# Performance work log

Hardware: AMD Instinct MI355X
Metric: run time of the kernel (lower is better)

The kernel has to match this reference:

```python
import jax, jax.numpy as jnp
import numpy as np

VOCAB, EMB, HID, TAG, T = 500000, 50, 50, 5, 4096  # HID = hidden_dim//2 per direction
START, STOP, NEG = 3, 4, -10000.0


def setup_inputs() -> dict:
    key = jax.random.key(0)
    ks = jax.random.split(key, 14)
    sentence = jax.random.randint(ks[0], (T,), 0, VOCAB, dtype=jnp.int32)
    embed = jax.random.normal(ks[1], (VOCAB, EMB), dtype=jnp.float32)
    # PyTorch LSTM params, gate order (i, f, g, o); b = b_ih + b_hh fused (same math)
    Wih_f = jax.random.normal(ks[2], (4 * HID, EMB), dtype=jnp.float32) * 0.1
    Whh_f = jax.random.normal(ks[3], (4 * HID, HID), dtype=jnp.float32) * 0.1
    b_f = jax.random.normal(ks[4], (4 * HID,), dtype=jnp.float32) * 0.1
    Wih_b = jax.random.normal(ks[5], (4 * HID, EMB), dtype=jnp.float32) * 0.1
    Whh_b = jax.random.normal(ks[6], (4 * HID, HID), dtype=jnp.float32) * 0.1
    b_b = jax.random.normal(ks[7], (4 * HID,), dtype=jnp.float32) * 0.1
    Wt = jax.random.normal(ks[8], (TAG, 2 * HID), dtype=jnp.float32) * 0.1
    bt = jax.random.normal(ks[9], (TAG,), dtype=jnp.float32) * 0.1
    transitions = jax.random.normal(ks[10], (TAG, TAG), dtype=jnp.float32)
    transitions = transitions.at[START, :].set(NEG).at[:, STOP].set(NEG)
    h0 = jax.random.normal(ks[11], (2, HID), dtype=jnp.float32)  # [fwd/bwd dir]
    c0 = jax.random.normal(ks[12], (2, HID), dtype=jnp.float32)
    return dict(sentence=sentence, embed=embed, Wih_f=Wih_f, Whh_f=Whh_f, b_f=b_f,
                Wih_b=Wih_b, Whh_b=Whh_b, b_b=b_b, Wt=Wt, bt=bt,
                transitions=transitions, h0=h0, c0=c0)


def _lstm_dir(x, h0, c0, Wih, Whh, b):
    # x: [T, EMB] -> hs: [T, HID]; PyTorch gate order i,f,g,o
    def step(carry, xt):
        h, c = carry
        z = xt @ Wih.T + h @ Whh.T + b  # [4H]
        i, f, g, o = jnp.split(z, 4)
        i, f, o = jax.nn.sigmoid(i), jax.nn.sigmoid(f), jax.nn.sigmoid(o)
        c = f * c + i * jnp.tanh(g)
        h = o * jnp.tanh(c)
        return (h, c), h
    _, hs = jax.lax.scan(step, (h0, c0), x)
    return hs


def _lstm_feats(sentence, embed, Wih_f, Whh_f, b_f, Wih_b, Whh_b, b_b, Wt, bt, h0, c0):
    x = embed[sentence]                       # [T, EMB]
    hf = _lstm_dir(x, h0[0], c0[0], Wih_f, Whh_f, b_f)            # [T, HID]
    hb = _lstm_dir(x[::-1], h0[1], c0[1], Wih_b, Whh_b, b_b)[::-1]  # [T, HID]
    h = jnp.concatenate([hf, hb], axis=-1)    # [T, 2*HID]
    return h @ Wt.T + bt                       # [T, TAG]


def reference(sentence, embed, Wih_f, Whh_f, b_f, Wih_b, Whh_b, b_b, Wt, bt, transitions, h0, c0):
    feats = _lstm_feats(sentence, embed, Wih_f, Whh_f, b_f, Wih_b, Whh_b, b_b, Wt, bt, h0, c0)

    fv0 = jnp.full((TAG,), NEG, dtype=feats.dtype).at[START].set(0.0)

    def vstep(fv, feat):
        m = fv[None, :] + transitions          # [next_tag, prev_tag]
        bp = jnp.argmax(m, axis=1)             # [TAG] best prev for each next
        fv_new = jnp.max(m, axis=1) + feat
        return fv_new, bp

    fv, bps = jax.lax.scan(vstep, fv0, feats)  # bps: [T, TAG]
    terminal = fv + transitions[STOP]
    last = jnp.argmax(terminal)

    def bt_step(tag, bp):
        return bp[tag], tag                    # carry prev tag, emit current tag

    _start, path = jax.lax.scan(bt_step, last, bps, reverse=True)
    score = terminal[last]
    return path.astype(jnp.int32), score
```

## Files before the change

kernel.cpp:

```cpp
#include <hip/hip_runtime.h>
#include <math.h>

#define EMB 50
#define HID 50
#define G4  200
#define NTAG 5
#define NEGV (-10000.0f)
#define TAG_START 3
#define TAG_STOP  4
#define T_MAX 4096
#define TB 8
#define WPAD 52

typedef float f32x4 __attribute__((ext_vector_type(4)));
typedef float f32x2 __attribute__((ext_vector_type(2)));

#define LO2(v) __builtin_shufflevector(v, v, 0, 1)
#define HI2(v) __builtin_shufflevector(v, v, 2, 3)

__global__ __launch_bounds__(256)
void k_embed_proj(const int* __restrict__ sent,
                  const float* __restrict__ embed,
                  const float* __restrict__ Wf, const float* __restrict__ bf,
                  const float* __restrict__ Wb, const float* __restrict__ bb,
                  float* __restrict__ pre, int T) {
  __shared__ __align__(16) float Wl[G4 * WPAD];
  __shared__ __align__(16) float xl[TB * WPAD];
  const int tid = threadIdx.x;
  const int t0  = blockIdx.x * TB;
  int ntt = T - t0; if (ntt > TB) ntt = TB;

  for (int e = tid; e < ntt * EMB; e += 256) {
    int tt = e / EMB, k = e - tt * EMB;
    xl[tt * WPAD + k] = embed[(long long)sent[t0 + tt] * EMB + k];
  }

  for (int ph = 0; ph < 2; ++ph) {
    const float* W = ph ? Wb : Wf;
    const float* b = ph ? bb : bf;
    __syncthreads();
    for (int e = tid; e < G4 * EMB; e += 256) {
      int r = e / EMB, k = e - r * EMB;
      Wl[r * WPAD + k] = W[e];
    }
    __syncthreads();
    float* outBase = pre + ((long long)ph * (T + 4) + 2) * G4;
    for (int o = tid; o < ntt * G4; o += 256) {
      int tt = o / G4, j = o - tt * G4;
      const float* wr_ = &Wl[j * WPAD];
      const float* xx  = &xl[tt * WPAD];
      f32x2 a2 = {0.f, 0.f};
#pragma unroll
      for (int k4 = 0; k4 < 12; ++k4) {
        f32x4 wv = *(const f32x4*)&wr_[4 * k4];
        f32x4 xv = *(const f32x4*)&xx[4 * k4];
        a2 += LO2(wv) * LO2(xv);
        a2 += HI2(wv) * HI2(xv);
      }
      a2.x += wr_[48] * xx[48];
      a2.y += wr_[49] * xx[49];
      float acc = b[j] + a2.x + a2.y;
      int unit = j % HID, gate = j / HID;
      outBase[(long long)(t0 + tt) * G4 + unit * 4 + gate] = acc;
    }
  }
}

#define DPP_XOR1(v) __int_as_float(__builtin_amdgcn_update_dpp(0, __float_as_int(v), 0xB1, 0xF, 0xF, true))
#define DPP_XOR2(v) __int_as_float(__builtin_amdgcn_update_dpp(0, __float_as_int(v), 0x4E, 0xF, 0xF, true))
#define DPP_XOR3(v) __int_as_float(__builtin_amdgcn_update_dpp(0, __float_as_int(v), 0x1B, 0xF, 0xF, true))

__device__ __forceinline__ float dot16(f32x4 w0, f32x4 w1, f32x4 w2, f32x4 w3,
                                       f32x4 x0, f32x4 x1, f32x4 x2, f32x4 x3) {
  f32x2 a = {0.f, 0.f}, b = {0.f, 0.f};
  a += LO2(w0) * LO2(x0);  b += HI2(w0) * HI2(x0);
  a += LO2(w1) * LO2(x1);  b += HI2(w1) * HI2(x1);
  a += LO2(w2) * LO2(x2);  b += HI2(w2) * HI2(x2);
  a += LO2(w3) * LO2(x3);  b += HI2(w3) * HI2(x3);
  return (a.x + b.x) + (a.y + b.y);
}

#define LSTM_STEP(HRbuf, HWbuf)                                              \
  {                                                                          \
    const float* HR = HRbuf;                                                 \
    float*       HW = HWbuf;                                                 \
    f32x4 mp = *(const f32x4*)pp;                                            \
    pp += sG4;                                                               \
    f32x4 x0 = *(const f32x4*)&HR[16 * q + 0];                               \
    f32x4 x1 = *(const f32x4*)&HR[16 * q + 4];                               \
    f32x4 x2 = *(const f32x4*)&HR[16 * q + 8];                               \
    f32x4 x3 = *(const f32x4*)&HR[16 * q + 12];                              \
    float pi = dot16(Wi0, Wi1, Wi2, Wi3, x0, x1, x2, x3);                    \
    float pf = dot16(Wf0, Wf1, Wf2, Wf3, x0, x1, x2, x3);                    \
    float pg = dot16(Wg0, Wg1, Wg2, Wg3, x0, x1, x2, x3);                    \
    float po = dot16(Wo0, Wo1, Wo2, Wo3, x0, x1, x2, x3);                    \
    pi += DPP_XOR1(pi); pi += DPP_XOR2(pi);                                  \
    pf += DPP_XOR1(pf); pf += DPP_XOR2(pf);                                  \
    pg += DPP_XOR1(pg); pg += DPP_XOR2(pg);                                  \
    po += DPP_XOR1(po); po += DPP_XOR2(po);                                  \
    float zi = cp.x + pi, zf = cp.y + pf, zg = cp.z + pg, zo = cp.w + po;    \
    float zq = (q == 0) ? zi : (q == 1) ? zf : (q == 2) ? zg : zo;           \
    float xs = (q == 2) ? 2.f * zq : zq;                                     \
    float eq = __expf(-xs);                                                  \
    float sg = __builtin_amdgcn_rcpf(1.f + eq);                              \
    float act = (q == 2) ? 2.f * sg - 1.f : sg;                              \
    float ga1 = DPP_XOR1(act);                                               \
    float ga2 = DPP_XOR2(act);                                               \
    float ga3 = DPP_XOR3(act);                                               \
    float iv = (q == 0) ? act : (q == 1) ? ga1 : (q == 2) ? ga2 : ga3;       \
    float fv = (q == 0) ? ga1 : (q == 1) ? act : (q == 2) ? ga3 : ga2;       \
    float gv = (q == 0) ? ga2 : (q == 1) ? ga3 : (q == 2) ? act : ga1;       \
    float ov = (q == 0) ? ga3 : (q == 1) ? ga2 : (q == 2) ? ga1 : act;       \
    c = fv * c + iv * gv;                                                    \
    float e2 = __expf(-2.f * c);                                             \
    float tc = 2.f * __builtin_amdgcn_rcpf(1.f + e2) - 1.f;                  \
    float h = ov * tc;                                                       \
    if (wr) {                                                                \
      HW[jq] = h;                                                            \
      *hsp = h;                                                              \
    }                                                                        \
    asm volatile("s_waitcnt lgkmcnt(0)\n\ts_barrier" ::: "memory");          \
    hsp += sH;                                                               \
    cp = np; np = mp;                                                        \
  }

__global__ __launch_bounds__(256)
__attribute__((amdgpu_waves_per_eu(1, 1)))
void k_lstm(const float* __restrict__ pre,
            const float* __restrict__ Whh_f,
            const float* __restrict__ Whh_b,
            const float* __restrict__ h0, const float* __restrict__ c0,
            float* __restrict__ hs, int T) {
  const int d   = blockIdx.x;
  const int tid = threadIdx.x;
  const int j   = tid >> 2;
  const int q   = tid & 3;
  const int jq  = (j < HID) ? j : 0;
  const bool wr = (q == 0) && (j < HID);
  const float* __restrict__ Whh  = d ? Whh_b : Whh_f;
  const float* __restrict__ preD = pre + ((long long)d * (T + 4) + 2) * G4;

  __shared__ __align__(16) float hA[64];
  __shared__ __align__(16) float hB[64];

  const float* p0 = Whh + (long long)(0 * HID + jq) * HID + 16 * q;
  const float* p1 = Whh + (long long)(1 * HID + jq) * HID + 16 * q;
  const float* p2 = Whh + (long long)(2 * HID + jq) * HID + 16 * q;
  const float* p3 = Whh + (long long)(3 * HID + jq) * HID + 16 * q;
  f32x4 Wi0, Wi1, Wi2, Wi3, Wf0, Wf1, Wf2, Wf3;
  f32x4 Wg0, Wg1, Wg2, Wg3, Wo0, Wo1, Wo2, Wo3;
  asm volatile(
      "global_load_dwordx4 %0,  %16, off\n\t"
      "global_load_dwordx4 %1,  %16, off offset:16\n\t"
      "global_load_dwordx4 %2,  %16, off offset:32\n\t"
      "global_load_dwordx4 %3,  %16, off offset:48\n\t"
      "global_load_dwordx4 %4,  %17, off\n\t"
      "global_load_dwordx4 %5,  %17, off offset:16\n\t"
      "global_load_dwordx4 %6,  %17, off offset:32\n\t"
      "global_load_dwordx4 %7,  %17, off offset:48\n\t"
      "global_load_dwordx4 %8,  %18, off\n\t"
      "global_load_dwordx4 %9,  %18, off offset:16\n\t"
      "global_load_dwordx4 %10, %18, off offset:32\n\t"
      "global_load_dwordx4 %11, %18, off offset:48\n\t"
      "global_load_dwordx4 %12, %19, off\n\t"
      "global_load_dwordx4 %13, %19, off offset:16\n\t"
      "global_load_dwordx4 %14, %19, off offset:32\n\t"
      "global_load_dwordx4 %15, %19, off offset:48\n\t"
      "s_waitcnt vmcnt(0)"
      : "=&v"(Wi0), "=&v"(Wi1), "=&v"(Wi2), "=&v"(Wi3),
        "=&v"(Wf0), "=&v"(Wf1), "=&v"(Wf2), "=&v"(Wf3),
        "=&v"(Wg0), "=&v"(Wg1), "=&v"(Wg2), "=&v"(Wg3),
        "=&v"(Wo0), "=&v"(Wo1), "=&v"(Wo2), "=&v"(Wo3)
      : "v"(p0), "v"(p1), "v"(p2), "v"(p3));

  if (q == 3) {
    const f32x4 z4 = {0.f, 0.f, 0.f, 0.f};
    Wi0.z = 0.f; Wi0.w = 0.f; Wi1 = z4; Wi2 = z4; Wi3 = z4;
    Wf0.z = 0.f; Wf0.w = 0.f; Wf1 = z4; Wf2 = z4; Wf3 = z4;
    Wg0.z = 0.f; Wg0.w = 0.f; Wg1 = z4; Wg2 = z4; Wg3 = z4;
    Wo0.z = 0.f; Wo0.w = 0.f; Wo1 = z4; Wo2 = z4; Wo3 = z4;
  }

  float c = c0[d * HID + jq];
  if (tid < 64) { hA[tid] = 0.f; hB[tid] = 0.f; }
  __syncthreads();
  if (wr) hA[jq] = h0[d * HID + jq];
  __syncthreads();

  const int s = d ? -1 : 1;
  const int t0 = d ? (T - 1) : 0;
  const long long sG4 = (long long)s * G4;
  const long long sH  = (long long)s * (2 * HID);

  f32x4 cp = *(const f32x4*)&preD[(long long)t0 * G4 + 4 * jq];
  f32x4 np = *(const f32x4*)&preD[(long long)(t0 + s) * G4 + 4 * jq];
  const float* pp = preD + (long long)(t0 + 2 * s) * G4 + 4 * jq;
  float* hsp = hs + (long long)t0 * (2 * HID) + d * HID + jq;

  for (int it = 0; it < T; it += 2) {
    LSTM_STEP(hA, hB)
    LSTM_STEP(hB, hA)
  }
}

__global__ void k_feats(const float* __restrict__ hs, const float* __restrict__ Wt,
                        const float* __restrict__ bt, float* __restrict__ feats, int T) {
  int g = blockIdx.x * blockDim.x + threadIdx.x;
  if (g >= T * NTAG) return;
  int t = g / NTAG, m = g % NTAG;
  const float* h = hs + (long long)t * (2 * HID);
  const float* w = Wt + m * (2 * HID);
  float a = bt[m];
#pragma unroll
  for (int k = 0; k < 2 * HID; ++k) a += w[k] * h[k];
  feats[g] = a;
}

__global__ __launch_bounds__(64, 1)
void k_vchunk(const float* __restrict__ feats,
              const float* __restrict__ trans,
              float* __restrict__ fvh, float* __restrict__ misc,
              float* __restrict__ out, int T) {
  const int lane = threadIdx.x;
  const int L    = T >> 6;
  const int c0   = lane * L;

  __shared__ float Pl[64][26];

  float tr[NTAG * NTAG];
#pragma unroll
  for (int i = 0; i < NTAG * NTAG; ++i) tr[i] = trans[i];

  float P[25];
  {
    float ft[5];
#pragma unroll
    for (int k = 0; k < 5; ++k) ft[k] = feats[c0 * 5 + k];
#pragma unroll
    for (int n = 0; n < 5; ++n)
#pragma unroll
      for (int p = 0; p < 5; ++p) P[n * 5 + p] = tr[n * 5 + p] + ft[n];
  }
  for (int i = 1; i < L; ++i) {
    int t = c0 + i;
    float ft[5];
#pragma unroll
    for (int k = 0; k < 5; ++k) ft[k] = feats[t * 5 + k];
    float NP[25];
#pragma unroll
    for (int n = 0; n < 5; ++n) {
#pragma unroll
      for (int p = 0; p < 5; ++p) {
        float m = tr[n * 5 + 0] + P[0 + p];
        m = fmaxf(m, tr[n * 5 + 1] + P[5 + p]);
        m = fmaxf(m, tr[n * 5 + 2] + P[10 + p]);
        m = fmaxf(m, tr[n * 5 + 3] + P[15 + p]);
        m = fmaxf(m, tr[n * 5 + 4] + P[20 + p]);
        NP[n * 5 + p] = m + ft[n];
      }
    }
#pragma unroll
    for (int e = 0; e < 25; ++e) P[e] = NP[e];
  }
#pragma unroll
  for (int e = 0; e < 25; ++e) Pl[lane][e] = P[e];
  __syncthreads();

  float v0 = NEGV, v1 = NEGV, v2 = NEGV, v3 = 0.f, v4 = NEGV;
  float s0 = 0.f, s1 = 0.f, s2 = 0.f, s3 = 0.f, s4 = 0.f;
  for (int cc = 0; cc < 64; ++cc) {
    bool mine = (cc == lane);
    s0 = mine ? v0 : s0; s1 = mine ? v1 : s1; s2 = mine ? v2 : s2;
    s3 = mine ? v3 : s3; s4 = mine ? v4 : s4;
    float nv[5];
#pragma unroll
    for (int n = 0; n < 5; ++n) {
      float m = Pl[cc][n * 5 + 0] + v0;
      m = fmaxf(m, Pl[cc][n * 5 + 1] + v1);
      m = fmaxf(m, Pl[cc][n * 5 + 2] + v2);
      m = fmaxf(m, Pl[cc][n * 5 + 3] + v3);
      m = fmaxf(m, Pl[cc][n * 5 + 4] + v4);
      nv[n] = m;
    }
    v0 = nv[0]; v1 = nv[1]; v2 = nv[2]; v3 = nv[3]; v4 = nv[4];
  }

  float f0 = s0, f1 = s1, f2 = s2, f3 = s3, f4 = s4;
  for (int i = 0; i < L; ++i) {
    int t = c0 + i;
    fvh[t * 5 + 0] = f0; fvh[t * 5 + 1] = f1; fvh[t * 5 + 2] = f2;
    fvh[t * 5 + 3] = f3; fvh[t * 5 + 4] = f4;
    float ft0 = feats[t * 5 + 0], ft1 = feats[t * 5 + 1], ft2 = feats[t * 5 + 2];
    float ft3 = feats[t * 5 + 3], ft4 = feats[t * 5 + 4];
    float n0 = fmaxf(fmaxf(fmaxf(f0 + tr[0],  f1 + tr[1]),  fmaxf(f2 + tr[2],  f3 + tr[3])),  f4 + tr[4])  + ft0;
    float n1 = fmaxf(fmaxf(fmaxf(f0 + tr[5],  f1 + tr[6]),  fmaxf(f2 + tr[7],  f3 + tr[8])),  f4 + tr[9])  + ft1;
    float n2 = fmaxf(fmaxf(fmaxf(f0 + tr[10], f1 + tr[11]), fmaxf(f2 + tr[12], f3 + tr[13])), f4 + tr[14]) + ft2;
    float n3 = fmaxf(fmaxf(fmaxf(f0 + tr[15], f1 + tr[16]), fmaxf(f2 + tr[17], f3 + tr[18])), f4 + tr[19]) + ft3;
    float n4 = fmaxf(fmaxf(fmaxf(f0 + tr[20], f1 + tr[21]), fmaxf(f2 + tr[22], f3 + tr[23])), f4 + tr[24]) + ft4;
    f0 = n0; f1 = n1; f2 = n2; f3 = n3; f4 = n4;
  }

  if (lane == 63) {
    float b0 = f0 + tr[TAG_STOP * 5 + 0], b1 = f1 + tr[TAG_STOP * 5 + 1];
    float b2 = f2 + tr[TAG_STOP * 5 + 2], b3 = f3 + tr[TAG_STOP * 5 + 3];
    float b4 = f4 + tr[TAG_STOP * 5 + 4];
    int last = 0; float best = b0;
    if (b1 > best) { best = b1; last = 1; }
    if (b2 > best) { best = b2; last = 2; }
    if (b3 > best) { best = b3; last = 3; }
    if (b4 > best) { best = b4; last = 4; }
    out[T] = best; misc[0] = (float)last;
  }
}

__global__ __launch_bounds__(1024) void k_vbt(const float* __restrict__ trans,
                        const float* __restrict__ fvh, const float* __restrict__ misc,
                        float* __restrict__ out, int T) {
  __shared__ unsigned int bufA[T_MAX];
  __shared__ unsigned int bufB[T_MAX];
  int tid = threadIdx.x;

  {
    float tr[NTAG * NTAG];
#pragma unroll
    for (int i = 0; i < NTAG * NTAG; ++i) tr[i] = trans[i];
    for (int t = tid; t < T; t += 1024) {
      unsigned pack;
      if (t == T - 1) {
        pack = 0u | (1u << 3) | (2u << 6) | (3u << 9) | (4u << 12);
      } else {
        const float* fv = fvh + (long long)(t + 1) * 5;
        float g0 = fv[0], g1 = fv[1], g2 = fv[2], g3 = fv[3], g4 = fv[4];
        pack = 0u;
#pragma unroll
        for (int nx = 0; nx < NTAG; ++nx) {
          float v0 = g0 + tr[nx * 5 + 0], v1 = g1 + tr[nx * 5 + 1], v2 = g2 + tr[nx * 5 + 2];
          float v3 = g3 + tr[nx * 5 + 3], v4 = g4 + tr[nx * 5 + 4];
          int bi = 0; float bv = v0;
          if (v1 > bv) { bv = v1; bi = 1; }
          if (v2 > bv) { bv = v2; bi = 2; }
          if (v3 > bv) { bv = v3; bi = 3; }
          if (v4 > bv) { bv = v4; bi = 4; }
          pack |= (unsigned)bi << (3 * nx);
        }
      }
      bufA[t] = pack;
    }
  }
  __syncthreads();

  unsigned int* cur = bufA;
  unsigned int* nxt = bufB;
  for (int dstep = 1; dstep < T; dstep <<= 1) {
    for (int t = tid; t < T; t += 1024) {
      unsigned v = cur[t];
      int u = t + dstep;
      if (u < T) {
        unsigned qq_ = cur[u];
        unsigned r = 0u;
#pragma unroll
        for (int x = 0; x < NTAG; ++x) {
          unsigned qs = (qq_ >> (3 * x)) & 7u;
          unsigned pp = (v >> (3 * qs)) & 7u;
          r |= pp << (3 * x);
        }
        v = r;
      }
      nxt[t] = v;
    }
    __syncthreads();
    unsigned int* tmp = cur; cur = nxt; nxt = tmp;
  }

  int last = (int)misc[0];
  for (int t = tid; t < T; t += 1024) {
    out[t] = (float)((cur[t] >> (3 * last)) & 7u);
  }
}

extern "C" void kernel_launch(void* const* d_in, const int* in_sizes, int n_in,
                              void* d_out, int out_size, void* d_ws, size_t ws_size,
                              hipStream_t stream) {
  const int*   sent  = (const int*)  d_in[0];
  const float* embed = (const float*)d_in[1];
  const float* Wih_f = (const float*)d_in[2];
  const float* Whh_f = (const float*)d_in[3];
  const float* b_f   = (const float*)d_in[4];
  const float* Wih_b = (const float*)d_in[5];
  const float* Whh_b = (const float*)d_in[6];
  const float* b_b   = (const float*)d_in[7];
  const float* Wt    = (const float*)d_in[8];
  const float* bt    = (const float*)d_in[9];
  const float* trans = (const float*)d_in[10];
  const float* h0    = (const float*)d_in[11];
  const float* c0    = (const float*)d_in[12];
  int T = in_sizes[0];

  float* out = (float*)d_out;
  float* pre   = (float*)d_ws;
  float* hs    = pre + 2 * (size_t)(T + 4) * G4;
  float* feats = hs + (size_t)T * 2 * HID;
  float* fvh   = feats + (size_t)T * NTAG;
  float* misc  = fvh + (size_t)(T + 1) * NTAG;

  k_embed_proj<<<(T + TB - 1) / TB, 256, 0, stream>>>(sent, embed, Wih_f, b_f, Wih_b, b_b, pre, T);
  k_lstm<<<2, 256, 0, stream>>>(pre, Whh_f, Whh_b, h0, c0, hs, T);
  k_feats<<<(T * NTAG + 255) / 256, 256, 0, stream>>>(hs, Wt, bt, feats, T);
  k_vchunk<<<1, 64, 0, stream>>>(feats, trans, fvh, misc, out, T);
  k_vbt<<<1, 1024, 0, stream>>>(trans, fvh, misc, out, T);
}
```

Measured before the change: 1.425 ms.

## Run each LSTM direction in a single wavefront, dropping barriers and DPP reductions

The recurrent LSTM kernel moves from 256 threads, with four lanes per hidden unit joined by DPP reductions and an s_barrier every step, to a single 64-lane wavefront. In the new layout each lane holds all four full 50-wide weight rows in registers and computes every gate itself. Because the whole block is one wave, the shared h vector is written and read with no hardware barrier. The per-step gate exchange and the tanh of the g gate are simplified as well, reusing exp(-z) squared. In exchange each lane does about four times more multiply-adds per step and needs many more registers.

```diff
diff --git a/kernel.cpp b/kernel.cpp
--- a/kernel.cpp
+++ b/kernel.cpp
@@ -66,140 +66,106 @@
   }
 }
 
-#define DPP_XOR1(v) __int_as_float(__builtin_amdgcn_update_dpp(0, __float_as_int(v), 0xB1, 0xF, 0xF, true))
-#define DPP_XOR2(v) __int_as_float(__builtin_amdgcn_update_dpp(0, __float_as_int(v), 0x4E, 0xF, 0xF, true))
-#define DPP_XOR3(v) __int_as_float(__builtin_amdgcn_update_dpp(0, __float_as_int(v), 0x1B, 0xF, 0xF, true))
-
-__device__ __forceinline__ float dot16(f32x4 w0, f32x4 w1, f32x4 w2, f32x4 w3,
-                                       f32x4 x0, f32x4 x1, f32x4 x2, f32x4 x3) {
-  f32x2 a = {0.f, 0.f}, b = {0.f, 0.f};
-  a += LO2(w0) * LO2(x0);  b += HI2(w0) * HI2(x0);
-  a += LO2(w1) * LO2(x1);  b += HI2(w1) * HI2(x1);
-  a += LO2(w2) * LO2(x2);  b += HI2(w2) * HI2(x2);
-  a += LO2(w3) * LO2(x3);  b += HI2(w3) * HI2(x3);
-  return (a.x + b.x) + (a.y + b.y);
-}
-
-#define LSTM_STEP(HRbuf, HWbuf)                                              \
-  {                                                                          \
-    const float* HR = HRbuf;                                                 \
-    float*       HW = HWbuf;                                                 \
-    f32x4 mp = *(const f32x4*)pp;                                            \
-    pp += sG4;                                                               \
-    f32x4 x0 = *(const f32x4*)&HR[16 * q + 0];                               \
-    f32x4 x1 = *(const f32x4*)&HR[16 * q + 4];                               \
-    f32x4 x2 = *(const f32x4*)&HR[16 * q + 8];                               \
-    f32x4 x3 = *(const f32x4*)&HR[16 * q + 12];                              \
-    float pi = dot16(Wi0, Wi1, Wi2, Wi3, x0, x1, x2, x3);                    \
-    float pf = dot16(Wf0, Wf1, Wf2, Wf3, x0, x1, x2, x3);                    \
-    float pg = dot16(Wg0, Wg1, Wg2, Wg3, x0, x1, x2, x3);                    \
-    float po = dot16(Wo0, Wo1, Wo2, Wo3, x0, x1, x2, x3);                    \
-    pi += DPP_XOR1(pi); pi += DPP_XOR2(pi);                                  \
-    pf += DPP_XOR1(pf); pf += DPP_XOR2(pf);                                  \
-    pg += DPP_XOR1(pg); pg += DPP_XOR2(pg);                                  \
-    po += DPP_XOR1(po); po += DPP_XOR2(po);                                  \
-    float zi = cp.x + pi, zf = cp.y + pf, zg = cp.z + pg, zo = cp.w + po;    \
-    float zq = (q == 0) ? zi : (q == 1) ? zf : (q == 2) ? zg : zo;           \
-    float xs = (q == 2) ? 2.f * zq : zq;                                     \
-    float eq = __expf(-xs);                                                  \
-    float sg = __builtin_amdgcn_rcpf(1.f + eq);                              \
-    float act = (q == 2) ? 2.f * sg - 1.f : sg;                              \
-    float ga1 = DPP_XOR1(act);                                               \
-    float ga2 = DPP_XOR2(act);                                               \
-    float ga3 = DPP_XOR3(act);                                               \
-    float iv = (q == 0) ? act : (q == 1) ? ga1 : (q == 2) ? ga2 : ga3;       \
-    float fv = (q == 0) ? ga1 : (q == 1) ? act : (q == 2) ? ga3 : ga2;       \
-    float gv = (q == 0) ? ga2 : (q == 1) ? ga3 : (q == 2) ? act : ga1;       \
-    float ov = (q == 0) ? ga3 : (q == 1) ? ga2 : (q == 2) ? ga1 : act;       \
-    c = fv * c + iv * gv;                                                    \
-    float e2 = __expf(-2.f * c);                                             \
-    float tc = 2.f * __builtin_amdgcn_rcpf(1.f + e2) - 1.f;                  \
-    float h = ov * tc;                                                       \
-    if (wr) {                                                                \
-      HW[jq] = h;                                                            \
-      *hsp = h;                                                              \
-    }                                                                        \
-    asm volatile("s_waitcnt lgkmcnt(0)\n\ts_barrier" ::: "memory");          \
-    hsp += sH;                                                               \
-    cp = np; np = mp;                                                        \
-  }
-
-__global__ __launch_bounds__(256)
+#define WLOAD(P, base)                                                        \
+  f32x4 P##0, P##1, P##2, P##3, P##4, P##5, P##6, P##7, P##8, P##9, P##10, P##11; \
+  f32x2 P##T_;                                                                \
+  asm volatile(                                                               \
+      "global_load_dwordx4 %0, %13, off\n\t"                                  \
+      "global_load_dwordx4 %1, %13, off offset:16\n\t"                        \
+      "global_load_dwordx4 %2, %13, off offset:32\n\t"                        \
+      "global_load_dwordx4 %3, %13, off offset:48\n\t"                        \
+      "global_load_dwordx4 %4, %13, off offset:64\n\t"                        \
+      "global_load_dwordx4 %5, %13, off offset:80\n\t"                        \
+      "global_load_dwordx4 %6, %13, off offset:96\n\t"                        \
+      "global_load_dwordx4 %7, %13, off offset:112\n\t"                       \
+      "global_load_dwordx4 %8, %13, off offset:128\n\t"                       \
+      "global_load_dwordx4 %9, %13, off offset:144\n\t"                       \
+      "global_load_dwordx4 %10, %13, off offset:160\n\t"                      \
+      "global_load_dwordx4 %11, %13, off offset:176\n\t"                      \
+      "global_load_dwordx2 %12, %13, off offset:192\n\t"                      \
+      "s_waitcnt vmcnt(0)"                                                    \
+      : "=&v"(P##0), "=&v"(P##1), "=&v"(P##2), "=&v"(P##3), "=&v"(P##4),      \
+        "=&v"(P##5), "=&v"(P##6), "=&v"(P##7), "=&v"(P##8), "=&v"(P##9),      \
+        "=&v"(P##10), "=&v"(P##11), "=&v"(P##T_)                              \
+      : "v"(base));
+
+#define CHUNK(K)                                                              \
+  { f32x4 xx = *(const f32x4*)&hL[4 * K];                                     \
+    Ai += LO2(Wi##K) * LO2(xx); Bi += HI2(Wi##K) * HI2(xx);                   \
+    Af += LO2(Wf##K) * LO2(xx); Bf += HI2(Wf##K) * HI2(xx);                   \
+    Ag += LO2(Wg##K) * LO2(xx); Bg += HI2(Wg##K) * HI2(xx);                   \
+    Ao += LO2(Wo##K) * LO2(xx); Bo += HI2(Wo##K) * HI2(xx); }
+
+__global__ __launch_bounds__(64)
 __attribute__((amdgpu_waves_per_eu(1, 1)))
 void k_lstm(const float* __restrict__ pre,
             const float* __restrict__ Whh_f,
             const float* __restrict__ Whh_b,
             const float* __restrict__ h0, const float* __restrict__ c0,
             float* __restrict__ hs, int T) {
-  const int d   = blockIdx.x;
-  const int tid = threadIdx.x;
-  const int j   = tid >> 2;
-  const int q   = tid & 3;
-  const int jq  = (j < HID) ? j : 0;
-  const bool wr = (q == 0) && (j < HID);
+  const int d    = blockIdx.x;
+  const int lane = threadIdx.x;
+  const int j    = (lane < HID) ? lane : 0;
+  const bool wr  = (lane < HID);
   const float* __restrict__ Whh  = d ? Whh_b : Whh_f;
   const float* __restrict__ preD = pre + ((long long)d * (T + 4) + 2) * G4;
 
-  __shared__ __align__(16) float hA[64];
-  __shared__ __align__(16) float hB[64];
-
-  const float* p0 = Whh + (long long)(0 * HID + jq) * HID + 16 * q;
-  const float* p1 = Whh + (long long)(1 * HID + jq) * HID + 16 * q;
-  const float* p2 = Whh + (long long)(2 * HID + jq) * HID + 16 * q;
-  const float* p3 = Whh + (long long)(3 * HID + jq) * HID + 16 * q;
-  f32x4 Wi0, Wi1, Wi2, Wi3, Wf0, Wf1, Wf2, Wf3;
-  f32x4 Wg0, Wg1, Wg2, Wg3, Wo0, Wo1, Wo2, Wo3;
-  asm volatile(
-      "global_load_dwordx4 %0,  %16, off\n\t"
-      "global_load_dwordx4 %1,  %16, off offset:16\n\t"
-      "global_load_dwordx4 %2,  %16, off offset:32\n\t"
-      "global_load_dwordx4 %3,  %16, off offset:48\n\t"
-      "global_load_dwordx4 %4,  %17, off\n\t"
-      "global_load_dwordx4 %5,  %17, off offset:16\n\t"
-      "global_load_dwordx4 %6,  %17, off offset:32\n\t"
-      "global_load_dwordx4 %7,  %17, off offset:48\n\t"
-      "global_load_dwordx4 %8,  %18, off\n\t"
-      "global_load_dwordx4 %9,  %18, off offset:16\n\t"
-      "global_load_dwordx4 %10, %18, off offset:32\n\t"
-      "global_load_dwordx4 %11, %18, off offset:48\n\t"
-      "global_load_dwordx4 %12, %19, off\n\t"
-      "global_load_dwordx4 %13, %19, off offset:16\n\t"
-      "global_load_dwordx4 %14, %19, off offset:32\n\t"
-      "global_load_dwordx4 %15, %19, off offset:48\n\t"
-      "s_waitcnt vmcnt(0)"
-      : "=&v"(Wi0), "=&v"(Wi1), "=&v"(Wi2), "=&v"(Wi3),
-        "=&v"(Wf0), "=&v"(Wf1), "=&v"(Wf2), "=&v"(Wf3),
-        "=&v"(Wg0), "=&v"(Wg1), "=&v"(Wg2), "=&v"(Wg3),
-        "=&v"(Wo0), "=&v"(Wo1), "=&v"(Wo2), "=&v"(Wo3)
-      : "v"(p0), "v"(p1), "v"(p2), "v"(p3));
-
-  if (q == 3) {
-    const f32x4 z4 = {0.f, 0.f, 0.f, 0.f};
-    Wi0.z = 0.f; Wi0.w = 0.f; Wi1 = z4; Wi2 = z4; Wi3 = z4;
-    Wf0.z = 0.f; Wf0.w = 0.f; Wf1 = z4; Wf2 = z4; Wf3 = z4;
-    Wg0.z = 0.f; Wg0.w = 0.f; Wg1 = z4; Wg2 = z4; Wg3 = z4;
-    Wo0.z = 0.f; Wo0.w = 0.f; Wo1 = z4; Wo2 = z4; Wo3 = z4;
-  }
-
-  float c = c0[d * HID + jq];
-  if (tid < 64) { hA[tid] = 0.f; hB[tid] = 0.f; }
+  __shared__ __align__(16) float hL[WPAD];
+
+  WLOAD(Wi, Whh + (long long)(0 * HID + j) * HID)
+  WLOAD(Wf, Whh + (long long)(1 * HID + j) * HID)
+  WLOAD(Wg, Whh + (long long)(2 * HID + j) * HID)
+  WLOAD(Wo, Whh + (long long)(3 * HID + j) * HID)
+
+  float c = c0[d * HID + j];
+  if (wr) hL[lane] = h0[d * HID + lane];
+  if (lane >= HID && lane < WPAD) hL[lane] = 0.f;
   __syncthreads();
-  if (wr) hA[jq] = h0[d * HID + jq];
-  __syncthreads();
-
-  const int s = d ? -1 : 1;
+
+  const int s  = d ? -1 : 1;
   const int t0 = d ? (T - 1) : 0;
   const long long sG4 = (long long)s * G4;
   const long long sH  = (long long)s * (2 * HID);
 
-  f32x4 cp = *(const f32x4*)&preD[(long long)t0 * G4 + 4 * jq];
-  f32x4 np = *(const f32x4*)&preD[(long long)(t0 + s) * G4 + 4 * jq];
-  const float* pp = preD + (long long)(t0 + 2 * s) * G4 + 4 * jq;
-  float* hsp = hs + (long long)t0 * (2 * HID) + d * HID + jq;
-
-  for (int it = 0; it < T; it += 2) {
-    LSTM_STEP(hA, hB)
-    LSTM_STEP(hB, hA)
+  f32x4 cp = *(const f32x4*)&preD[(long long)t0 * G4 + 4 * j];
+  f32x4 np = *(const f32x4*)&preD[(long long)(t0 + s) * G4 + 4 * j];
+  const float* pp = preD + (long long)(t0 + 2 * s) * G4 + 4 * j;
+  float* hsp = hs + (long long)t0 * (2 * HID) + d * HID + j;
+
+  for (int it = 0; it < T; ++it) {
+    f32x4 mp = *(const f32x4*)pp;
+    pp += sG4;
+    f32x2 Ai = {0.f, 0.f}, Bi = {0.f, 0.f};
+    f32x2 Af = {0.f, 0.f}, Bf = {0.f, 0.f};
+    f32x2 Ag = {0.f, 0.f}, Bg = {0.f, 0.f};
+    f32x2 Ao = {0.f, 0.f}, Bo = {0.f, 0.f};
+    CHUNK(0) CHUNK(1) CHUNK(2) CHUNK(3) CHUNK(4)  CHUNK(5)
+    CHUNK(6) CHUNK(7) CHUNK(8) CHUNK(9) CHUNK(10) CHUNK(11)
+    {
+      f32x2 xt = *(const f32x2*)&hL[48];
+      Ai += WiT_ * xt; Af += WfT_ * xt; Ag += WgT_ * xt; Ao += WoT_ * xt;
+    }
+    float zi = cp.x + ((Ai.x + Ai.y) + (Bi.x + Bi.y));
+    float zf = cp.y + ((Af.x + Af.y) + (Bf.x + Bf.y));
+    float zg = cp.z + ((Ag.x + Ag.y) + (Bg.x + Bg.y));
+    float zo = cp.w + ((Ao.x + Ao.y) + (Bo.x + Bo.y));
+    float ei  = __expf(-zi), ef2 = __expf(-zf);
+    float eg2 = __expf(-zg), eo2 = __expf(-zo);
+    float si = __builtin_amdgcn_rcpf(1.f + ei);
+    float sf = __builtin_amdgcn_rcpf(1.f + ef2);
+    float so = __builtin_amdgcn_rcpf(1.f + eo2);
+    float tg = 2.f * __builtin_amdgcn_rcpf(1.f + eg2 * eg2) - 1.f;
+    c = sf * c + si * tg;
+    float e2 = __expf(-2.f * c);
+    float tc = 2.f * __builtin_amdgcn_rcpf(1.f + e2) - 1.f;
+    float h = so * tc;
+    if (wr) {
+      hL[j] = h;
+      *hsp = h;
+    }
+    asm volatile("" ::: "memory");
+    hsp += sH;
+    cp = np; np = mp;
   }
 }
 
@@ -404,7 +370,7 @@
   float* misc  = fvh + (size_t)(T + 1) * NTAG;
 
   k_embed_proj<<<(T + TB - 1) / TB, 256, 0, stream>>>(sent, embed, Wih_f, b_f, Wih_b, b_b, pre, T);
-  k_lstm<<<2, 256, 0, stream>>>(pre, Whh_f, Whh_b, h0, c0, hs, T);
+  k_lstm<<<2, 64, 0, stream>>>(pre, Whh_f, Whh_b, h0, c0, hs, T);
   k_feats<<<(T * NTAG + 255) / 256, 256, 0, stream>>>(hs, Wt, bt, feats, T);
   k_vchunk<<<1, 64, 0, stream>>>(feats, trans, fvh, misc, out, T);
   k_vbt<<<1, 1024, 0, stream>>>(trans, fvh, misc, out, T);
```

New measurement: 2.698 ms. +89.4%, slower.
